# Kernel optimization log

Measured on AMD Instinct MI355X. Metric: run time of the kernel, lower is better.

Reference implementation:

```python
import jax, jax.numpy as jnp
import numpy as np

N_NODES = 50000
N_EDGES = 800000
NODE_IN = 128
NODE_OUT = 64
EDGE_IN = 64
EDGE_OUT = 64
NEG_SLOPE = 0.01  # torch F.leaky_relu default


def setup_inputs() -> dict:
    key = jax.random.key(0)
    k = jax.random.split(key, 6)
    h = jax.random.normal(k[0], (N_NODES, NODE_IN), dtype=jnp.float32)
    e = jax.random.normal(k[1], (N_EDGES, EDGE_IN), dtype=jnp.float32)
    # Linear weights (bias=False), scaled roughly like torch default init
    Wn = jax.random.normal(k[2], (NODE_OUT, NODE_IN), dtype=jnp.float32) * (1.0 / np.sqrt(NODE_IN))
    We = jax.random.normal(k[3], (EDGE_OUT, EDGE_IN), dtype=jnp.float32) * (1.0 / np.sqrt(EDGE_IN))
    Wa = jax.random.normal(k[4], (1, EDGE_OUT + NODE_OUT), dtype=jnp.float32) * (1.0 / np.sqrt(EDGE_OUT + NODE_OUT))
    src = jax.random.randint(k[5], (N_EDGES,), 0, N_NODES, dtype=jnp.int32)
    return {"h": h, "e": e, "Wn": Wn, "We": We, "Wa": Wa, "src": src}


def reference(h, e, Wn, We, Wa, src):
    n_nodes = h.shape[0]
    node_feat = h @ Wn.T                         # [N, node_out] = fc_n(h)
    e_w = e @ We.T                               # [E, edge_out] = fc_e(e)
    src_ft = node_feat[src]                      # gather src node features per edge
    z2 = jnp.concatenate([e_w, src_ft], axis=-1) # [E, edge_out+node_out] (edge first, as in module)
    a = z2 @ Wa.T                                # [E, 1] attention logit
    e_lr = jnp.where(a >= 0, a, NEG_SLOPE * a)   # leaky_relu
    # segment softmax over edges grouped by src node (group_apply_edges softmax dim=1)
    m = jax.ops.segment_max(e_lr, src, num_segments=n_nodes)     # [N, 1]
    ex = jnp.exp(e_lr - m[src])
    denom = jax.ops.segment_sum(ex, src, num_segments=n_nodes)   # [N, 1]
    gamma = ex / denom[src]                      # [E, 1]
    e_weighted = gamma * e_w                     # [E, edge_out]
    return node_feat, e_weighted
```

## Files before the change

### kernel.cpp

```cpp
#include <hip/hip_runtime.h>


constexpr int kNodes   = 50000;
constexpr int kEdges   = 800000;
constexpr int kNodeIn  = 128;
constexpr int kNodeOut = 64;
constexpr int kEdgeIn  = 64;
constexpr int kEdgeOut = 64;
#define NEG_SLOPE 0.01f

typedef __attribute__((ext_vector_type(8))) short short8;
typedef __attribute__((ext_vector_type(4))) short short4v;
typedef __attribute__((ext_vector_type(4))) float f32x4;

constexpr int kOffV     = 0;
constexpr int kOffSn    = 64;
constexpr int kOffDenom = 50064;
constexpr int kOffEx    = 100064;
constexpr int kOffWeB   = 900064;
constexpr int kOffWnB   = 902112;
constexpr int kOffEbf   = 906240;

__device__ inline short f2bf(float x) {
    union { float f; unsigned u; } v; v.f = x;
    unsigned r = v.u + 0x7FFFu + ((v.u >> 16) & 1u);
    return (short)(r >> 16);
}

__global__ void k0_prep(const float* __restrict__ We, const float* __restrict__ Wn,
                        const float* __restrict__ Wa,
                        float* __restrict__ v, short* __restrict__ Web,
                        short* __restrict__ Wnb) {
    int b = blockIdx.x, t = threadIdx.x;
    if (b == 0 && t < kEdgeIn) {
        float acc = 0.f;
        #pragma unroll
        for (int c = 0; c < kEdgeOut; ++c) acc = fmaf(Wa[c], We[c * kEdgeIn + t], acc);
        v[t] = acc;
    }
    if (b < 16) {
        int i = b * 256 + t;
        Web[i] = f2bf(We[i]);
    } else {
        int i = (b - 16) * 256 + t;
        Wnb[i] = f2bf(Wn[i]);
    }
}

__global__ __launch_bounds__(256) void k1_mfma(
    const float* __restrict__ h, const short* __restrict__ Wnb,
    const float* __restrict__ Wa, float* __restrict__ node_feat,
    float* __restrict__ s_n, float* __restrict__ denom) {
    const int lane = threadIdx.x & 63;
    const int l15  = lane & 15;
    const int lhi  = lane >> 4;
    const int n0   = blockIdx.x * 64 + (threadIdx.x >> 6) * 16;

    int gid = blockIdx.x * 256 + threadIdx.x;
    if (gid < kNodes) denom[gid] = 0.f;

    short8 Bf[4][4];
    #pragma unroll
    for (int kt = 0; kt < 4; ++kt)
        #pragma unroll
        for (int ct = 0; ct < 4; ++ct)
            Bf[kt][ct] = *reinterpret_cast<const short8*>(
                Wnb + (ct * 16 + l15) * kNodeIn + kt * 32 + lhi * 8);

    const int  arow   = n0 + l15;
    const bool avalid = arow < kNodes;
    const float* hrow = h + (size_t)arow * kNodeIn;

    f32x4 acc[4];
    #pragma unroll
    for (int ct = 0; ct < 4; ++ct) acc[ct] = (f32x4)(0.f);

    #pragma unroll
    for (int kt = 0; kt < 4; ++kt) {
        short8 af;
        if (avalid) {
            f32x4 t0 = __builtin_nontemporal_load(
                reinterpret_cast<const f32x4*>(hrow + kt * 32 + lhi * 8));
            f32x4 t1 = __builtin_nontemporal_load(
                reinterpret_cast<const f32x4*>(hrow + kt * 32 + lhi * 8 + 4));
            af[0] = f2bf(t0[0]); af[1] = f2bf(t0[1]); af[2] = f2bf(t0[2]); af[3] = f2bf(t0[3]);
            af[4] = f2bf(t1[0]); af[5] = f2bf(t1[1]); af[6] = f2bf(t1[2]); af[7] = f2bf(t1[3]);
        } else {
            #pragma unroll
            for (int j = 0; j < 8; ++j) af[j] = 0;
        }
        #pragma unroll
        for (int ct = 0; ct < 4; ++ct)
            acc[ct] = __builtin_amdgcn_mfma_f32_16x16x32_bf16(af, Bf[kt][ct], acc[ct], 0, 0, 0);
    }

    float wa[4];
    #pragma unroll
    for (int ct = 0; ct < 4; ++ct) wa[ct] = Wa[64 + ct * 16 + l15];

    #pragma unroll
    for (int reg = 0; reg < 4; ++reg) {
        int r = n0 + lhi * 4 + reg;
        bool rv = r < kNodes;
        float part = 0.f;
        #pragma unroll
        for (int ct = 0; ct < 4; ++ct) part = fmaf(wa[ct], acc[ct][reg], part);
        if (rv) {
            #pragma unroll
            for (int ct = 0; ct < 4; ++ct)
                __builtin_nontemporal_store(acc[ct][reg],
                    node_feat + (size_t)r * kNodeOut + ct * 16 + l15);
        }
        part += __shfl_xor(part, 1, 64);
        part += __shfl_xor(part, 2, 64);
        part += __shfl_xor(part, 4, 64);
        part += __shfl_xor(part, 8, 64);
        if (rv && l15 == 0) s_n[r] = part;
    }
}

__global__ __launch_bounds__(256) void kconv(
    const float* __restrict__ e, const float* __restrict__ v,
    const int* __restrict__ src, const float* __restrict__ s_n,
    float* __restrict__ denom, float* __restrict__ ex,
    short* __restrict__ ebf) {
    const int t   = threadIdx.x;
    const int q   = t & 15;
    const int rlo = t >> 4;
    const long base = (long)blockIdx.x * 64;

    f32x4 vv = *(reinterpret_cast<const f32x4*>(v) + q);

    #pragma unroll
    for (int it = 0; it < 4; ++it) {
        long r = base + it * 16 + rlo;
        f32x4 d = __builtin_nontemporal_load(
            reinterpret_cast<const f32x4*>(e + r * kEdgeIn) + q);
        float part = d[0] * vv[0] + d[1] * vv[1] + d[2] * vv[2] + d[3] * vv[3];
        part += __shfl_xor(part, 1, 64);
        part += __shfl_xor(part, 2, 64);
        part += __shfl_xor(part, 4, 64);
        part += __shfl_xor(part, 8, 64);
        short4v o;
        o[0] = f2bf(d[0]); o[1] = f2bf(d[1]); o[2] = f2bf(d[2]); o[3] = f2bf(d[3]);
        *reinterpret_cast<short4v*>(ebf + r * kEdgeIn + q * 4) = o;
        if (q == 0) {
            int s = src[r];
            float a = part + s_n[s];
            float lr = (a >= 0.f) ? a : NEG_SLOPE * a;
            float xe = __expf(lr);
            ex[r] = xe;
            atomicAdd(denom + s, xe);
        }
    }
}

__global__ __launch_bounds__(256) void k4_mfma(
    const short* __restrict__ ebf, const short* __restrict__ Web,
    const int* __restrict__ src, const float* __restrict__ denom,
    const float* __restrict__ ex, float* __restrict__ oute) {
    const int wave = threadIdx.x >> 6;
    const int lane = threadIdx.x & 63;
    const int l15  = lane & 15;
    const int lhi  = lane >> 4;
    const long base = (long)blockIdx.x * 256 + wave * 64;

    short8 Bf[2][4];
    #pragma unroll
    for (int kt = 0; kt < 2; ++kt)
        #pragma unroll
        for (int ct = 0; ct < 4; ++ct)
            Bf[kt][ct] = *reinterpret_cast<const short8*>(
                Web + (ct * 16 + l15) * kEdgeIn + kt * 32 + lhi * 8);

    f32x4 acc[4][4];
    #pragma unroll
    for (int m = 0; m < 4; ++m)
        #pragma unroll
        for (int n = 0; n < 4; ++n) acc[m][n] = (f32x4)(0.f);

    #pragma unroll
    for (int m = 0; m < 4; ++m) {
        const short* erow = ebf + (base + m * 16 + l15) * kEdgeIn;
        #pragma unroll
        for (int kt = 0; kt < 2; ++kt) {
            short8 af = *reinterpret_cast<const short8*>(erow + kt * 32 + lhi * 8);
            #pragma unroll
            for (int ct = 0; ct < 4; ++ct)
                acc[m][ct] = __builtin_amdgcn_mfma_f32_16x16x32_bf16(
                    af, Bf[kt][ct], acc[m][ct], 0, 0, 0);
        }
    }

    #pragma unroll
    for (int m = 0; m < 4; ++m) {
        const long r0 = base + m * 16 + lhi * 4;
        float4 exv = *reinterpret_cast<const float4*>(ex + r0);
        int4   sv  = *reinterpret_cast<const int4*>(src + r0);
        float ga[4];
        ga[0] = exv.x * __builtin_amdgcn_rcpf(denom[sv.x]);
        ga[1] = exv.y * __builtin_amdgcn_rcpf(denom[sv.y]);
        ga[2] = exv.z * __builtin_amdgcn_rcpf(denom[sv.z]);
        ga[3] = exv.w * __builtin_amdgcn_rcpf(denom[sv.w]);
        #pragma unroll
        for (int reg = 0; reg < 4; ++reg) {
            float gv = ga[reg];
            #pragma unroll
            for (int ct = 0; ct < 4; ++ct)
                __builtin_nontemporal_store(acc[m][ct][reg] * gv,
                    oute + (r0 + reg) * kEdgeOut + ct * 16 + l15);
        }
    }
}

extern "C" void kernel_launch(void* const* d_in, const int* in_sizes, int n_in,
                              void* d_out, int out_size, void* d_ws, size_t ws_size,
                              hipStream_t stream) {
    const float* h   = (const float*)d_in[0];
    const float* e   = (const float*)d_in[1];
    const float* Wn  = (const float*)d_in[2];
    const float* We  = (const float*)d_in[3];
    const float* Wa  = (const float*)d_in[4];
    const int*   src = (const int*)d_in[5];

    float* node_feat = (float*)d_out;
    float* oute      = (float*)d_out + (size_t)kNodes * kNodeOut;

    float* ws    = (float*)d_ws;
    float* v     = ws + kOffV;
    float* s_n   = ws + kOffSn;
    float* denom = ws + kOffDenom;
    float* ex    = ws + kOffEx;
    short* Web   = (short*)(ws + kOffWeB);
    short* Wnb   = (short*)(ws + kOffWnB);
    short* ebf   = (short*)(ws + kOffEbf);

    k0_prep<<<48, 256, 0, stream>>>(We, Wn, Wa, v, Web, Wnb);
    k1_mfma<<<(kNodes + 63) / 64, 256, 0, stream>>>(h, Wnb, Wa, node_feat, s_n, denom);
    kconv<<<kEdges / 64, 256, 0, stream>>>(e, v, src, s_n, denom, ex, ebf);
    k4_mfma<<<kEdges / 256, 256, 0, stream>>>(ebf, Web, src, denom, ex, oute);
}
```

Before: 156.6 us.

## Privatize denominator atomics into 8 replicas and swap MFMA operands for vector stores

The edge kernel now spreads its per-node exp-sum atomics across 8 replicated denominator arrays, chosen by block index, and a new reduction kernel sums them afterwards. The goal is to cut atomic contention on the same addresses. In both MFMA kernels the weight and data operands are swapped, so each lane holds 4 consecutive output columns of one row. Outputs are then written as 16-byte vector stores, and the gamma/src/ex loads become one per lane. The cost is an extra launch, zeroing 8x more buffer, and extra reduction traffic.

```diff
diff --git a/kernel.cpp b/kernel.cpp
--- a/kernel.cpp
+++ b/kernel.cpp
@@ -7,6 +7,7 @@
 constexpr int kNodeOut = 64;
 constexpr int kEdgeIn  = 64;
 constexpr int kEdgeOut = 64;
+constexpr int kNodesP  = 50016;
 #define NEG_SLOPE 0.01f
 
 typedef __attribute__((ext_vector_type(8))) short short8;
@@ -16,10 +17,12 @@
 constexpr int kOffV     = 0;
 constexpr int kOffSn    = 64;
 constexpr int kOffDenom = 50064;
-constexpr int kOffEx    = 100064;
-constexpr int kOffWeB   = 900064;
-constexpr int kOffWnB   = 902112;
-constexpr int kOffEbf   = 906240;
+constexpr int kOffRep   = 100064;
+constexpr int kOffEx    = 500192;
+constexpr int kOffWeB   = 1300192;
+constexpr int kOffWnB   = 1302240;
+constexpr int kOffEbf   = 1306368;
+constexpr int kRepTotal = 8 * kNodesP;
 
 __device__ inline short f2bf(float x) {
     union { float f; unsigned u; } v; v.f = x;
@@ -50,25 +53,27 @@
 __global__ __launch_bounds__(256) void k1_mfma(
     const float* __restrict__ h, const short* __restrict__ Wnb,
     const float* __restrict__ Wa, float* __restrict__ node_feat,
-    float* __restrict__ s_n, float* __restrict__ denom) {
+    float* __restrict__ s_n, float* __restrict__ rep) {
     const int lane = threadIdx.x & 63;
     const int l15  = lane & 15;
     const int lhi  = lane >> 4;
     const int n0   = blockIdx.x * 64 + (threadIdx.x >> 6) * 16;
 
     int gid = blockIdx.x * 256 + threadIdx.x;
-    if (gid < kNodes) denom[gid] = 0.f;
-
-    short8 Bf[4][4];
+    if (gid < kRepTotal) rep[gid] = 0.f;
+    int g2 = gid + 200192;
+    if (g2 < kRepTotal) rep[g2] = 0.f;
+
+    short8 Af[4][4];
     #pragma unroll
     for (int kt = 0; kt < 4; ++kt)
         #pragma unroll
         for (int ct = 0; ct < 4; ++ct)
-            Bf[kt][ct] = *reinterpret_cast<const short8*>(
+            Af[kt][ct] = *reinterpret_cast<const short8*>(
                 Wnb + (ct * 16 + l15) * kNodeIn + kt * 32 + lhi * 8);
 
     const int  arow   = n0 + l15;
-    const bool avalid = arow < kNodes;
+    const bool rv     = arow < kNodes;
     const float* hrow = h + (size_t)arow * kNodeIn;
 
     f32x4 acc[4];
@@ -77,57 +82,50 @@
 
     #pragma unroll
     for (int kt = 0; kt < 4; ++kt) {
-        short8 af;
-        if (avalid) {
+        short8 bf;
+        if (rv) {
             f32x4 t0 = __builtin_nontemporal_load(
                 reinterpret_cast<const f32x4*>(hrow + kt * 32 + lhi * 8));
             f32x4 t1 = __builtin_nontemporal_load(
                 reinterpret_cast<const f32x4*>(hrow + kt * 32 + lhi * 8 + 4));
-            af[0] = f2bf(t0[0]); af[1] = f2bf(t0[1]); af[2] = f2bf(t0[2]); af[3] = f2bf(t0[3]);
-            af[4] = f2bf(t1[0]); af[5] = f2bf(t1[1]); af[6] = f2bf(t1[2]); af[7] = f2bf(t1[3]);
+            bf[0] = f2bf(t0[0]); bf[1] = f2bf(t0[1]); bf[2] = f2bf(t0[2]); bf[3] = f2bf(t0[3]);
+            bf[4] = f2bf(t1[0]); bf[5] = f2bf(t1[1]); bf[6] = f2bf(t1[2]); bf[7] = f2bf(t1[3]);
         } else {
             #pragma unroll
-            for (int j = 0; j < 8; ++j) af[j] = 0;
+            for (int j = 0; j < 8; ++j) bf[j] = 0;
         }
         #pragma unroll
         for (int ct = 0; ct < 4; ++ct)
-            acc[ct] = __builtin_amdgcn_mfma_f32_16x16x32_bf16(af, Bf[kt][ct], acc[ct], 0, 0, 0);
-    }
-
-    float wa[4];
-    #pragma unroll
-    for (int ct = 0; ct < 4; ++ct) wa[ct] = Wa[64 + ct * 16 + l15];
-
-    #pragma unroll
-    for (int reg = 0; reg < 4; ++reg) {
-        int r = n0 + lhi * 4 + reg;
-        bool rv = r < kNodes;
-        float part = 0.f;
-        #pragma unroll
-        for (int ct = 0; ct < 4; ++ct) part = fmaf(wa[ct], acc[ct][reg], part);
-        if (rv) {
-            #pragma unroll
-            for (int ct = 0; ct < 4; ++ct)
-                __builtin_nontemporal_store(acc[ct][reg],
-                    node_feat + (size_t)r * kNodeOut + ct * 16 + l15);
-        }
-        part += __shfl_xor(part, 1, 64);
-        part += __shfl_xor(part, 2, 64);
-        part += __shfl_xor(part, 4, 64);
-        part += __shfl_xor(part, 8, 64);
-        if (rv && l15 == 0) s_n[r] = part;
-    }
+            acc[ct] = __builtin_amdgcn_mfma_f32_16x16x32_bf16(Af[kt][ct], bf, acc[ct], 0, 0, 0);
+    }
+
+    float part = 0.f;
+    #pragma unroll
+    for (int ct = 0; ct < 4; ++ct) {
+        f32x4 wa4 = *reinterpret_cast<const f32x4*>(Wa + 64 + ct * 16 + lhi * 4);
+        part = fmaf(wa4[0], acc[ct][0], part);
+        part = fmaf(wa4[1], acc[ct][1], part);
+        part = fmaf(wa4[2], acc[ct][2], part);
+        part = fmaf(wa4[3], acc[ct][3], part);
+        if (rv)
+            __builtin_nontemporal_store(acc[ct],
+                reinterpret_cast<f32x4*>(node_feat + (size_t)arow * kNodeOut + ct * 16 + lhi * 4));
+    }
+    part += __shfl_xor(part, 16, 64);
+    part += __shfl_xor(part, 32, 64);
+    if (rv && lhi == 0) s_n[arow] = part;
 }
 
 __global__ __launch_bounds__(256) void kconv(
     const float* __restrict__ e, const float* __restrict__ v,
     const int* __restrict__ src, const float* __restrict__ s_n,
-    float* __restrict__ denom, float* __restrict__ ex,
+    float* __restrict__ rep, float* __restrict__ ex,
     short* __restrict__ ebf) {
     const int t   = threadIdx.x;
     const int q   = t & 15;
     const int rlo = t >> 4;
     const long base = (long)blockIdx.x * 64;
+    float* myrep = rep + (blockIdx.x & 7) * kNodesP;
 
     f32x4 vv = *(reinterpret_cast<const f32x4*>(v) + q);
 
@@ -150,9 +148,19 @@
             float lr = (a >= 0.f) ? a : NEG_SLOPE * a;
             float xe = __expf(lr);
             ex[r] = xe;
-            atomicAdd(denom + s, xe);
-        }
-    }
+            atomicAdd(myrep + s, xe);
+        }
+    }
+}
+
+__global__ __launch_bounds__(256) void kred(
+    const float* __restrict__ rep, float* __restrict__ denom) {
+    int i = blockIdx.x * 256 + threadIdx.x;
+    if (i >= kNodes) return;
+    float s = 0.f;
+    #pragma unroll
+    for (int x = 0; x < 8; ++x) s += rep[x * kNodesP + i];
+    denom[i] = s;
 }
 
 __global__ __launch_bounds__(256) void k4_mfma(
@@ -165,12 +173,12 @@
     const int lhi  = lane >> 4;
     const long base = (long)blockIdx.x * 256 + wave * 64;
 
-    short8 Bf[2][4];
+    short8 Af[2][4];
     #pragma unroll
     for (int kt = 0; kt < 2; ++kt)
         #pragma unroll
         for (int ct = 0; ct < 4; ++ct)
-            Bf[kt][ct] = *reinterpret_cast<const short8*>(
+            Af[kt][ct] = *reinterpret_cast<const short8*>(
                 Web + (ct * 16 + l15) * kEdgeIn + kt * 32 + lhi * 8);
 
     f32x4 acc[4][4];
@@ -184,31 +192,24 @@
         const short* erow = ebf + (base + m * 16 + l15) * kEdgeIn;
         #pragma unroll
         for (int kt = 0; kt < 2; ++kt) {
-            short8 af = *reinterpret_cast<const short8*>(erow + kt * 32 + lhi * 8);
+            short8 bf = *reinterpret_cast<const short8*>(erow + kt * 32 + lhi * 8);
             #pragma unroll
             for (int ct = 0; ct < 4; ++ct)
                 acc[m][ct] = __builtin_amdgcn_mfma_f32_16x16x32_bf16(
-                    af, Bf[kt][ct], acc[m][ct], 0, 0, 0);
+                    Af[kt][ct], bf, acc[m][ct], 0, 0, 0);
         }
     }
 
     #pragma unroll
     for (int m = 0; m < 4; ++m) {
-        const long r0 = base + m * 16 + lhi * 4;
-        float4 exv = *reinterpret_cast<const float4*>(ex + r0);
-        int4   sv  = *reinterpret_cast<const int4*>(src + r0);
-        float ga[4];
-        ga[0] = exv.x * __builtin_amdgcn_rcpf(denom[sv.x]);
-        ga[1] = exv.y * __builtin_amdgcn_rcpf(denom[sv.y]);
-        ga[2] = exv.z * __builtin_amdgcn_rcpf(denom[sv.z]);
-        ga[3] = exv.w * __builtin_amdgcn_rcpf(denom[sv.w]);
-        #pragma unroll
-        for (int reg = 0; reg < 4; ++reg) {
-            float gv = ga[reg];
-            #pragma unroll
-            for (int ct = 0; ct < 4; ++ct)
-                __builtin_nontemporal_store(acc[m][ct][reg] * gv,
-                    oute + (r0 + reg) * kEdgeOut + ct * 16 + l15);
+        const long edge = base + m * 16 + l15;
+        int s = src[edge];
+        float g = ex[edge] * __builtin_amdgcn_rcpf(denom[s]);
+        #pragma unroll
+        for (int ct = 0; ct < 4; ++ct) {
+            f32x4 o = acc[m][ct] * g;
+            __builtin_nontemporal_store(o,
+                reinterpret_cast<f32x4*>(oute + edge * kEdgeOut + ct * 16 + lhi * 4));
         }
     }
 }
@@ -230,13 +231,15 @@
     float* v     = ws + kOffV;
     float* s_n   = ws + kOffSn;
     float* denom = ws + kOffDenom;
+    float* rep   = ws + kOffRep;
     float* ex    = ws + kOffEx;
     short* Web   = (short*)(ws + kOffWeB);
     short* Wnb   = (short*)(ws + kOffWnB);
     short* ebf   = (short*)(ws + kOffEbf);
 
     k0_prep<<<48, 256, 0, stream>>>(We, Wn, Wa, v, Web, Wnb);
-    k1_mfma<<<(kNodes + 63) / 64, 256, 0, stream>>>(h, Wnb, Wa, node_feat, s_n, denom);
-    kconv<<<kEdges / 64, 256, 0, stream>>>(e, v, src, s_n, denom, ex, ebf);
+    k1_mfma<<<(kNodes + 63) / 64, 256, 0, stream>>>(h, Wnb, Wa, node_feat, s_n, rep);
+    kconv<<<kEdges / 64, 256, 0, stream>>>(e, v, src, s_n, rep, ex, ebf);
+    kred<<<(kNodes + 255) / 256, 256, 0, stream>>>(rep, denom);
     k4_mfma<<<kEdges / 256, 256, 0, stream>>>(ebf, Web, src, denom, ex, oute);
 }
```

Measured after the change: 163.5 us. +4.4%, slower.

## Fuse edge GEMM with attention logit and store unnormalized bf16 products

Applied to the files above, without the earlier changes.

The edge conversion kernel and the edge GEMM are merged. Each wave now converts e to bf16 in registers, runs the MFMA (transposed so each lane holds one edge's outputs), computes the attention logit from the GEMM result, and writes exp-weighted products as bf16 to a workspace buffer. A light scale kernel then multiplies by the reciprocal softmax denominator and writes the fp32 output. This removes the separate ex buffer and the precomputed Wa·We vector, and drops nontemporal loads on h. The cost is an extra bf16 rounding of the weighted output and more redundant src/s_n loads per lane.

```diff
diff --git a/kernel.cpp b/kernel.cpp
--- a/kernel.cpp
+++ b/kernel.cpp
@@ -13,31 +13,26 @@
 typedef __attribute__((ext_vector_type(4))) short short4v;
 typedef __attribute__((ext_vector_type(4))) float f32x4;
 
-constexpr int kOffV     = 0;
-constexpr int kOffSn    = 64;
-constexpr int kOffDenom = 50064;
-constexpr int kOffEx    = 100064;
-constexpr int kOffWeB   = 900064;
-constexpr int kOffWnB   = 902112;
-constexpr int kOffEbf   = 906240;
+constexpr int kOffSn    = 0;
+constexpr int kOffDenom = 50048;
+constexpr int kOffWeB   = 100096;
+constexpr int kOffWnB   = 102144;
+constexpr int kOffUbf   = 106240;
 
 __device__ inline short f2bf(float x) {
     union { float f; unsigned u; } v; v.f = x;
     unsigned r = v.u + 0x7FFFu + ((v.u >> 16) & 1u);
     return (short)(r >> 16);
 }
+__device__ inline float bf2f(short x) {
+    union { unsigned u; float f; } v;
+    v.u = ((unsigned)(unsigned short)x) << 16;
+    return v.f;
+}
 
 __global__ void k0_prep(const float* __restrict__ We, const float* __restrict__ Wn,
-                        const float* __restrict__ Wa,
-                        float* __restrict__ v, short* __restrict__ Web,
-                        short* __restrict__ Wnb) {
+                        short* __restrict__ Web, short* __restrict__ Wnb) {
     int b = blockIdx.x, t = threadIdx.x;
-    if (b == 0 && t < kEdgeIn) {
-        float acc = 0.f;
-        #pragma unroll
-        for (int c = 0; c < kEdgeOut; ++c) acc = fmaf(Wa[c], We[c * kEdgeIn + t], acc);
-        v[t] = acc;
-    }
     if (b < 16) {
         int i = b * 256 + t;
         Web[i] = f2bf(We[i]);
@@ -79,10 +74,8 @@
     for (int kt = 0; kt < 4; ++kt) {
         short8 af;
         if (avalid) {
-            f32x4 t0 = __builtin_nontemporal_load(
-                reinterpret_cast<const f32x4*>(hrow + kt * 32 + lhi * 8));
-            f32x4 t1 = __builtin_nontemporal_load(
-                reinterpret_cast<const f32x4*>(hrow + kt * 32 + lhi * 8 + 4));
+            f32x4 t0 = *reinterpret_cast<const f32x4*>(hrow + kt * 32 + lhi * 8);
+            f32x4 t1 = *reinterpret_cast<const f32x4*>(hrow + kt * 32 + lhi * 8 + 4);
             af[0] = f2bf(t0[0]); af[1] = f2bf(t0[1]); af[2] = f2bf(t0[2]); af[3] = f2bf(t0[3]);
             af[4] = f2bf(t1[0]); af[5] = f2bf(t1[1]); af[6] = f2bf(t1[2]); af[7] = f2bf(t1[3]);
         } else {
@@ -119,98 +112,98 @@
     }
 }
 
-__global__ __launch_bounds__(256) void kconv(
-    const float* __restrict__ e, const float* __restrict__ v,
-    const int* __restrict__ src, const float* __restrict__ s_n,
-    float* __restrict__ denom, float* __restrict__ ex,
-    short* __restrict__ ebf) {
-    const int t   = threadIdx.x;
-    const int q   = t & 15;
-    const int rlo = t >> 4;
-    const long base = (long)blockIdx.x * 64;
-
-    f32x4 vv = *(reinterpret_cast<const f32x4*>(v) + q);
-
-    #pragma unroll
-    for (int it = 0; it < 4; ++it) {
-        long r = base + it * 16 + rlo;
-        f32x4 d = __builtin_nontemporal_load(
-            reinterpret_cast<const f32x4*>(e + r * kEdgeIn) + q);
-        float part = d[0] * vv[0] + d[1] * vv[1] + d[2] * vv[2] + d[3] * vv[3];
-        part += __shfl_xor(part, 1, 64);
-        part += __shfl_xor(part, 2, 64);
-        part += __shfl_xor(part, 4, 64);
-        part += __shfl_xor(part, 8, 64);
-        short4v o;
-        o[0] = f2bf(d[0]); o[1] = f2bf(d[1]); o[2] = f2bf(d[2]); o[3] = f2bf(d[3]);
-        *reinterpret_cast<short4v*>(ebf + r * kEdgeIn + q * 4) = o;
-        if (q == 0) {
-            int s = src[r];
-            float a = part + s_n[s];
-            float lr = (a >= 0.f) ? a : NEG_SLOPE * a;
-            float xe = __expf(lr);
-            ex[r] = xe;
-            atomicAdd(denom + s, xe);
-        }
-    }
-}
-
-__global__ __launch_bounds__(256) void k4_mfma(
-    const short* __restrict__ ebf, const short* __restrict__ Web,
-    const int* __restrict__ src, const float* __restrict__ denom,
-    const float* __restrict__ ex, float* __restrict__ oute) {
+__global__ __launch_bounds__(256) void kfused(
+    const float* __restrict__ e, const short* __restrict__ Web,
+    const float* __restrict__ Wa, const int* __restrict__ src,
+    const float* __restrict__ s_n, float* __restrict__ denom,
+    short* __restrict__ ubf) {
     const int wave = threadIdx.x >> 6;
     const int lane = threadIdx.x & 63;
     const int l15  = lane & 15;
     const int lhi  = lane >> 4;
     const long base = (long)blockIdx.x * 256 + wave * 64;
 
-    short8 Bf[2][4];
+    short8 Af[2][4];
     #pragma unroll
     for (int kt = 0; kt < 2; ++kt)
         #pragma unroll
         for (int ct = 0; ct < 4; ++ct)
-            Bf[kt][ct] = *reinterpret_cast<const short8*>(
+            Af[kt][ct] = *reinterpret_cast<const short8*>(
                 Web + (ct * 16 + l15) * kEdgeIn + kt * 32 + lhi * 8);
 
-    f32x4 acc[4][4];
-    #pragma unroll
-    for (int m = 0; m < 4; ++m)
-        #pragma unroll
-        for (int n = 0; n < 4; ++n) acc[m][n] = (f32x4)(0.f);
+    f32x4 wa4[4];
+    #pragma unroll
+    for (int ct = 0; ct < 4; ++ct)
+        wa4[ct] = *reinterpret_cast<const f32x4*>(Wa + ct * 16 + lhi * 4);
 
     #pragma unroll
     for (int m = 0; m < 4; ++m) {
-        const short* erow = ebf + (base + m * 16 + l15) * kEdgeIn;
-        #pragma unroll
-        for (int kt = 0; kt < 2; ++kt) {
-            short8 af = *reinterpret_cast<const short8*>(erow + kt * 32 + lhi * 8);
-            #pragma unroll
-            for (int ct = 0; ct < 4; ++ct)
-                acc[m][ct] = __builtin_amdgcn_mfma_f32_16x16x32_bf16(
-                    af, Bf[kt][ct], acc[m][ct], 0, 0, 0);
-        }
-    }
-
-    #pragma unroll
-    for (int m = 0; m < 4; ++m) {
-        const long r0 = base + m * 16 + lhi * 4;
-        float4 exv = *reinterpret_cast<const float4*>(ex + r0);
-        int4   sv  = *reinterpret_cast<const int4*>(src + r0);
-        float ga[4];
-        ga[0] = exv.x * __builtin_amdgcn_rcpf(denom[sv.x]);
-        ga[1] = exv.y * __builtin_amdgcn_rcpf(denom[sv.y]);
-        ga[2] = exv.z * __builtin_amdgcn_rcpf(denom[sv.z]);
-        ga[3] = exv.w * __builtin_amdgcn_rcpf(denom[sv.w]);
-        #pragma unroll
-        for (int reg = 0; reg < 4; ++reg) {
-            float gv = ga[reg];
-            #pragma unroll
-            for (int ct = 0; ct < 4; ++ct)
-                __builtin_nontemporal_store(acc[m][ct][reg] * gv,
-                    oute + (r0 + reg) * kEdgeOut + ct * 16 + l15);
-        }
-    }
+        const long edge = base + m * 16 + l15;
+        const float* erow = e + edge * kEdgeIn;
+
+        f32x4 t0 = *reinterpret_cast<const f32x4*>(erow + lhi * 8);
+        f32x4 t1 = *reinterpret_cast<const f32x4*>(erow + lhi * 8 + 4);
+        f32x4 t2 = *reinterpret_cast<const f32x4*>(erow + 32 + lhi * 8);
+        f32x4 t3 = *reinterpret_cast<const f32x4*>(erow + 32 + lhi * 8 + 4);
+        short8 bf0, bf1;
+        bf0[0] = f2bf(t0[0]); bf0[1] = f2bf(t0[1]); bf0[2] = f2bf(t0[2]); bf0[3] = f2bf(t0[3]);
+        bf0[4] = f2bf(t1[0]); bf0[5] = f2bf(t1[1]); bf0[6] = f2bf(t1[2]); bf0[7] = f2bf(t1[3]);
+        bf1[0] = f2bf(t2[0]); bf1[1] = f2bf(t2[1]); bf1[2] = f2bf(t2[2]); bf1[3] = f2bf(t2[3]);
+        bf1[4] = f2bf(t3[0]); bf1[5] = f2bf(t3[1]); bf1[6] = f2bf(t3[2]); bf1[7] = f2bf(t3[3]);
+
+        f32x4 acc[4];
+        #pragma unroll
+        for (int ct = 0; ct < 4; ++ct) acc[ct] = (f32x4)(0.f);
+        #pragma unroll
+        for (int ct = 0; ct < 4; ++ct)
+            acc[ct] = __builtin_amdgcn_mfma_f32_16x16x32_bf16(Af[0][ct], bf0, acc[ct], 0, 0, 0);
+        #pragma unroll
+        for (int ct = 0; ct < 4; ++ct)
+            acc[ct] = __builtin_amdgcn_mfma_f32_16x16x32_bf16(Af[1][ct], bf1, acc[ct], 0, 0, 0);
+
+        float part = 0.f;
+        #pragma unroll
+        for (int ct = 0; ct < 4; ++ct) {
+            part = fmaf(wa4[ct][0], acc[ct][0], part);
+            part = fmaf(wa4[ct][1], acc[ct][1], part);
+            part = fmaf(wa4[ct][2], acc[ct][2], part);
+            part = fmaf(wa4[ct][3], acc[ct][3], part);
+        }
+        part += __shfl_xor(part, 16, 64);
+        part += __shfl_xor(part, 32, 64);
+
+        int s = src[edge];
+        float a  = part + s_n[s];
+        float lr = (a >= 0.f) ? a : NEG_SLOPE * a;
+        float xe = __expf(lr);
+
+        #pragma unroll
+        for (int ct = 0; ct < 4; ++ct) {
+            f32x4 uv = acc[ct] * xe;
+            short4v o;
+            o[0] = f2bf(uv[0]); o[1] = f2bf(uv[1]); o[2] = f2bf(uv[2]); o[3] = f2bf(uv[3]);
+            *reinterpret_cast<short4v*>(ubf + edge * kEdgeOut + ct * 16 + lhi * 4) = o;
+        }
+        if (lhi == 0) atomicAdd(denom + s, xe);
+    }
+}
+
+__global__ __launch_bounds__(256) void kscale(
+    const short* __restrict__ ubf, const int* __restrict__ src,
+    const float* __restrict__ denom, float* __restrict__ oute) {
+    long c = (long)blockIdx.x * 256 + threadIdx.x;
+    long r = c >> 4;
+    int  q = (int)(c & 15);
+    short4v u4 = *reinterpret_cast<const short4v*>(ubf + r * kEdgeOut + q * 4);
+    int s = src[r];
+    float g = __builtin_amdgcn_rcpf(denom[s]);
+    f32x4 o;
+    o[0] = bf2f(u4[0]) * g;
+    o[1] = bf2f(u4[1]) * g;
+    o[2] = bf2f(u4[2]) * g;
+    o[3] = bf2f(u4[3]) * g;
+    __builtin_nontemporal_store(o,
+        reinterpret_cast<f32x4*>(oute + r * kEdgeOut + q * 4));
 }
 
 extern "C" void kernel_launch(void* const* d_in, const int* in_sizes, int n_in,
@@ -227,16 +220,14 @@
     float* oute      = (float*)d_out + (size_t)kNodes * kNodeOut;
 
     float* ws    = (float*)d_ws;
-    float* v     = ws + kOffV;
     float* s_n   = ws + kOffSn;
     float* denom = ws + kOffDenom;
-    float* ex    = ws + kOffEx;
     short* Web   = (short*)(ws + kOffWeB);
     short* Wnb   = (short*)(ws + kOffWnB);
-    short* ebf   = (short*)(ws + kOffEbf);
-
-    k0_prep<<<48, 256, 0, stream>>>(We, Wn, Wa, v, Web, Wnb);
+    short* ubf   = (short*)(ws + kOffUbf);
+
+    k0_prep<<<48, 256, 0, stream>>>(We, Wn, Web, Wnb);
     k1_mfma<<<(kNodes + 63) / 64, 256, 0, stream>>>(h, Wnb, Wa, node_feat, s_n, denom);
-    kconv<<<kEdges / 64, 256, 0, stream>>>(e, v, src, s_n, denom, ex, ebf);
-    k4_mfma<<<kEdges / 256, 256, 0, stream>>>(ebf, Web, src, denom, ex, oute);
-}
+    kfused<<<kEdges / 256, 256, 0, stream>>>(e, Web, Wa, src, s_n, denom, ubf);
+    kscale<<<(kEdges * (kEdgeOut / 4) + 255) / 256, 256, 0, stream>>>(ubf, src, denom, oute);
+}
```

Measured after the change: 159.4 us. Within noise of the previous version (+1.8%).
